# Performance work log

Measured on AMD Instinct MI355X. Metric: run time of the kernel, lower is better.

## Reference

```python
import jax, jax.numpy as jnp
import numpy as np

EPS = 1e-12
BETA = 3.0
N_TH = 21


def setup_inputs() -> dict:
    key = jax.random.key(0)
    k1, k2 = jax.random.split(key)
    N, C = 65536, 1000
    logits = jax.random.normal(k1, (N, C), dtype=jnp.float32)
    labels = jax.random.randint(k2, (N,), 0, C, dtype=jnp.int64)
    idx = jnp.arange(N, dtype=jnp.int64)
    return {"logits": logits, "labels": labels, "idx": idx, "type": 0}


def _forward(logits, labels):
    # probs / confidences / predictions
    probs = jax.nn.softmax(logits, axis=1)                      # [N, C]
    conf = jnp.max(probs, axis=1)                               # [N]
    preds = jnp.argmax(probs, axis=1)                           # [N]
    # predictive uncertainty (type == 0): entropy of softmax
    unc = -jnp.sum(probs * jnp.log(probs + EPS), axis=-1)       # [N]
    umin, umax = jnp.min(unc), jnp.max(unc)
    th = jnp.linspace(0.0, 1.0, N_TH, dtype=logits.dtype)       # [21]
    unc_th = umin + th * (umax - umin)                          # [21]

    acc = (labels == preds)                                     # [N] bool
    t_unc = jnp.tanh(unc)                                       # [N]
    certain = unc[None, :] <= unc_th[:, None]                   # [21, N]
    a = acc[None, :]

    zero = jnp.zeros((), logits.dtype)
    n_ac = jnp.sum(jnp.where(a & certain, conf * (1.0 - t_unc), zero), axis=1)
    n_au = jnp.sum(jnp.where(a & ~certain, conf * t_unc, zero), axis=1)
    n_ic = jnp.sum(jnp.where(~a & certain, (1.0 - conf) * (1.0 - t_unc), zero), axis=1)
    n_iu = jnp.sum(jnp.where(~a & ~certain, (1.0 - conf) * t_unc, zero), axis=1)

    avu = (n_ac + n_iu) / (n_ac + n_au + n_ic + n_iu + EPS)     # [21]
    # sklearn.metrics.auc == trapezoidal rule over (th, avu)
    auc_avu = 0.5 * jnp.sum((avu[1:] + avu[:-1]) * (th[1:] - th[:-1]))
    # original wraps auc in a fresh tensor -> no grad through the AvU branch
    avu_loss = -BETA * jnp.log(jax.lax.stop_gradient(auc_avu) + EPS)

    logp = jax.nn.log_softmax(logits, axis=1)                   # [N, C]
    ce = -jnp.mean(jnp.take_along_axis(logp, labels[:, None], axis=1))
    return (avu_loss + ce)[None]                                # [1], matches torch


def reference(logits, labels, idx, type) -> jnp.ndarray:
    del idx, type  # idx unused; type=0 path (predictive uncertainty)
    return _forward(logits, labels)
```

## Files before the change

### kernel.cpp

```cpp
#include <hip/hip_runtime.h>
#include <math.h>

#define NROWS 65536
#define NC    1000
#define NTH   21

__device__ __forceinline__ void upd_max(float v, int i, float& m, int& mi) {
    if (v > m) { m = v; mi = i; }
}

__global__ void k0_init(float* bins, float* ce_sum, unsigned* umin_b, unsigned* umax_b) {
    int i = threadIdx.x;
    if (i < 88) bins[i] = 0.f;
    if (i == 88) *ce_sum = 0.f;
    if (i == 89) *umin_b = 0x7f800000u;
    if (i == 90) *umax_b = 0u;
}

__global__ __launch_bounds__(256) void k1_rowstats(
        const float* __restrict__ logits, const int* __restrict__ labels,
        float* __restrict__ unc_o, float* __restrict__ confs_o, float* __restrict__ logp_o)
{
    const int wave = threadIdx.x >> 6;
    const int lane = threadIdx.x & 63;
    const int row  = (blockIdx.x << 2) + wave;
    const float4* rp = (const float4*)(logits + (size_t)row * NC);

    float4 r0 = rp[lane];
    float4 r1 = rp[lane + 64];
    float4 r2 = rp[lane + 128];
    float4 r3 = make_float4(-1e30f, -1e30f, -1e30f, -1e30f);
    if (lane < 250 - 192) r3 = rp[lane + 192];

    float m = -1e30f; int mi = 0;
    int b0 = lane << 2;
    upd_max(r0.x, b0 + 0, m, mi); upd_max(r0.y, b0 + 1, m, mi);
    upd_max(r0.z, b0 + 2, m, mi); upd_max(r0.w, b0 + 3, m, mi);
    int b1 = (lane + 64) << 2;
    upd_max(r1.x, b1 + 0, m, mi); upd_max(r1.y, b1 + 1, m, mi);
    upd_max(r1.z, b1 + 2, m, mi); upd_max(r1.w, b1 + 3, m, mi);
    int b2 = (lane + 128) << 2;
    upd_max(r2.x, b2 + 0, m, mi); upd_max(r2.y, b2 + 1, m, mi);
    upd_max(r2.z, b2 + 2, m, mi); upd_max(r2.w, b2 + 3, m, mi);
    int b3 = (lane + 192) << 2;
    upd_max(r3.x, b3 + 0, m, mi); upd_max(r3.y, b3 + 1, m, mi);
    upd_max(r3.z, b3 + 2, m, mi); upd_max(r3.w, b3 + 3, m, mi);

    #pragma unroll
    for (int off = 1; off < 64; off <<= 1) {
        float om = __shfl_xor(m, off, 64);
        int   oi = __shfl_xor(mi, off, 64);
        if (om > m || (om == m && oi < mi)) { m = om; mi = oi; }
    }

    float se = 0.f, sx = 0.f;
#define ACCUM(v) { float t_ = (v) - m; float e_ = __expf(t_); se += e_; sx = fmaf(e_, t_, sx); }
    ACCUM(r0.x) ACCUM(r0.y) ACCUM(r0.z) ACCUM(r0.w)
    ACCUM(r1.x) ACCUM(r1.y) ACCUM(r1.z) ACCUM(r1.w)
    ACCUM(r2.x) ACCUM(r2.y) ACCUM(r2.z) ACCUM(r2.w)
    ACCUM(r3.x) ACCUM(r3.y) ACCUM(r3.z) ACCUM(r3.w)
#undef ACCUM
    #pragma unroll
    for (int off = 1; off < 64; off <<= 1) {
        se += __shfl_xor(se, off, 64);
        sx += __shfl_xor(sx, off, 64);
    }

    float Z    = se;
    float logZ = logf(Z);
    float conf = 1.0f / Z;
    float uncv = logZ - sx / Z;

    int label = labels[row];
    int f4 = label >> 2, slot = label & 3, it = f4 >> 6;
    float4 q = (it == 0) ? r0 : (it == 1) ? r1 : (it == 2) ? r2 : r3;
    float cand = (slot == 0) ? q.x : (slot == 1) ? q.y : (slot == 2) ? q.z : q.w;
    float xl = __shfl(cand, f4 & 63, 64);

    if (lane == 0) {
        unc_o[row]   = uncv;
        confs_o[row] = (mi == label) ? conf : -conf;
        logp_o[row]  = (xl - m) - logZ;
    }
}

__global__ __launch_bounds__(256) void k2_reduce(
        const float* __restrict__ unc, const float* __restrict__ logp,
        float* ce_sum, unsigned* umin_b, unsigned* umax_b)
{
    float mn = 1e30f, mx = -1e30f, s = 0.f;
    for (int i = blockIdx.x * 256 + threadIdx.x; i < NROWS; i += 256 * gridDim.x) {
        float u = unc[i];
        mn = fminf(mn, u); mx = fmaxf(mx, u); s += logp[i];
    }
    #pragma unroll
    for (int off = 1; off < 64; off <<= 1) {
        mn = fminf(mn, __shfl_xor(mn, off, 64));
        mx = fmaxf(mx, __shfl_xor(mx, off, 64));
        s += __shfl_xor(s, off, 64);
    }
    __shared__ float smn[4], smx[4], ss[4];
    int wave = threadIdx.x >> 6;
    if ((threadIdx.x & 63) == 0) { smn[wave] = mn; smx[wave] = mx; ss[wave] = s; }
    __syncthreads();
    if (threadIdx.x == 0) {
        mn = fminf(fminf(smn[0], smn[1]), fminf(smn[2], smn[3]));
        mx = fmaxf(fmaxf(smx[0], smx[1]), fmaxf(smx[2], smx[3]));
        s  = ss[0] + ss[1] + ss[2] + ss[3];
        atomicAdd(ce_sum, s);
        atomicMin(umin_b, __float_as_uint(mn));
        atomicMax(umax_b, __float_as_uint(mx));
    }
}

__global__ __launch_bounds__(256) void k3_hist(
        const float* __restrict__ unc, const float* __restrict__ confs,
        const unsigned* __restrict__ umin_b, const unsigned* __restrict__ umax_b,
        float* __restrict__ bins)
{
    __shared__ float h[88];
    for (int i = threadIdx.x; i < 88; i += 256) h[i] = 0.f;
    __syncthreads();
    float umin = __uint_as_float(*umin_b);
    float umax = __uint_as_float(*umax_b);
    float du = umax - umin;

    int i = blockIdx.x * 256 + threadIdx.x;
    float u  = unc[i];
    float cs = confs[i];
    float conf = fabsf(cs);
    bool  acc  = cs > 0.f;
    float tu = tanhf(u);

    int b = NTH;
    #pragma unroll
    for (int t = NTH - 1; t >= 0; --t) {
        float th = umin + ((float)t * 0.05f) * du;
        if (u <= th) b = t;
    }
    float w = acc ? conf : (1.f - conf);
    int base = acc ? 0 : 44;
    atomicAdd(&h[base + b],       w * (1.f - tu));
    atomicAdd(&h[base + 22 + b],  w * tu);
    __syncthreads();
    for (int i2 = threadIdx.x; i2 < 88; i2 += 256) {
        float v = h[i2];
        if (v != 0.f) atomicAdd(&bins[i2], v);
    }
}

__global__ void k4_final(const float* __restrict__ bins, const float* __restrict__ ce_sum,
                         float* __restrict__ out)
{
    if (threadIdx.x != 0 || blockIdx.x != 0) return;
    float tot_au = 0.f, tot_iu = 0.f;
    for (int b = 0; b < 22; ++b) { tot_au += bins[22 + b]; tot_iu += bins[66 + b]; }
    float cac = 0.f, cau = 0.f, cic = 0.f, ciu = 0.f;
    float avu[NTH];
    for (int t = 0; t < NTH; ++t) {
        cac += bins[t]; cau += bins[22 + t]; cic += bins[44 + t]; ciu += bins[66 + t];
        float nac = cac, nau = tot_au - cau, nic = cic, niu = tot_iu - ciu;
        avu[t] = (nac + niu) / (nac + nau + nic + niu + 1e-12f);
    }
    float auc = 0.f;
    for (int t = 0; t + 1 < NTH; ++t) auc += 0.5f * (avu[t + 1] + avu[t]) * 0.05f;
    float avu_loss = -3.0f * logf(auc + 1e-12f);
    float ce = -(*ce_sum) / (float)NROWS;
    out[0] = avu_loss + ce;
}

extern "C" void kernel_launch(void* const* d_in, const int* in_sizes, int n_in,
                              void* d_out, int out_size, void* d_ws, size_t ws_size,
                              hipStream_t stream)
{
    const float* logits = (const float*)d_in[0];
    const int*   labels = (const int*)d_in[1];
    float* ws    = (float*)d_ws;
    float* unc   = ws;
    float* confs = ws + NROWS;
    float* logp  = ws + 2 * NROWS;
    float* bins  = ws + 3 * NROWS;
    float* ce_sum = bins + 88;
    unsigned* umin_b = (unsigned*)(ce_sum + 1);
    unsigned* umax_b = umin_b + 1;

    hipLaunchKernelGGL(k0_init, dim3(1), dim3(128), 0, stream, bins, ce_sum, umin_b, umax_b);
    hipLaunchKernelGGL(k1_rowstats, dim3(NROWS / 4), dim3(256), 0, stream,
                       logits, labels, unc, confs, logp);
    hipLaunchKernelGGL(k2_reduce, dim3(256), dim3(256), 0, stream,
                       unc, logp, ce_sum, umin_b, umax_b);
    hipLaunchKernelGGL(k3_hist, dim3(NROWS / 256), dim3(256), 0, stream,
                       unc, confs, umin_b, umax_b, bins);
    hipLaunchKernelGGL(k4_final, dim3(1), dim3(64), 0, stream,
                       bins, ce_sum, (float*)d_out);
}
```

Baseline: 370.2 us.

## Fold min/max/CE reduction into rowstats and drop global atomics and init kernel

Each rowstats block now writes its own min, max and CE partial, which removes the separate reduction kernel and the init kernel. The histogram kernel re-reduces the 16K block partials in every one of its 64 blocks and writes per-block histograms instead of using global atomics. The final kernel sums the CE partials and the histograms. This cuts the launch count from five to three and avoids atomic contention, at the cost of redundant partial reads in each histogram block.

```diff
diff --git a/kernel.cpp b/kernel.cpp
--- a/kernel.cpp
+++ b/kernel.cpp
@@ -1,25 +1,21 @@
 #include <hip/hip_runtime.h>
 #include <math.h>
 
-#define NROWS 65536
-#define NC    1000
-#define NTH   21
+#define NROWS   65536
+#define NC      1000
+#define NTH     21
+#define K1_BLKS (NROWS / 4)
+#define H_BLKS  64
+#define NBINS   22
 
 __device__ __forceinline__ void upd_max(float v, int i, float& m, int& mi) {
     if (v > m) { m = v; mi = i; }
 }
 
-__global__ void k0_init(float* bins, float* ce_sum, unsigned* umin_b, unsigned* umax_b) {
-    int i = threadIdx.x;
-    if (i < 88) bins[i] = 0.f;
-    if (i == 88) *ce_sum = 0.f;
-    if (i == 89) *umin_b = 0x7f800000u;
-    if (i == 90) *umax_b = 0u;
-}
-
 __global__ __launch_bounds__(256) void k1_rowstats(
         const float* __restrict__ logits, const int* __restrict__ labels,
-        float* __restrict__ unc_o, float* __restrict__ confs_o, float* __restrict__ logp_o)
+        float* __restrict__ unc_o, float* __restrict__ confs_o,
+        float* __restrict__ pmin, float* __restrict__ pmax, float* __restrict__ pce)
 {
     const int wave = threadIdx.x >> 6;
     const int lane = threadIdx.x & 63;
@@ -76,56 +72,61 @@
     float4 q = (it == 0) ? r0 : (it == 1) ? r1 : (it == 2) ? r2 : r3;
     float cand = (slot == 0) ? q.x : (slot == 1) ? q.y : (slot == 2) ? q.z : q.w;
     float xl = __shfl(cand, f4 & 63, 64);
-
+    float logp = (xl - m) - logZ;
+
+    __shared__ float s_u[4], s_lp[4];
     if (lane == 0) {
         unc_o[row]   = uncv;
         confs_o[row] = (mi == label) ? conf : -conf;
-        logp_o[row]  = (xl - m) - logZ;
-    }
-}
-
-__global__ __launch_bounds__(256) void k2_reduce(
-        const float* __restrict__ unc, const float* __restrict__ logp,
-        float* ce_sum, unsigned* umin_b, unsigned* umax_b)
-{
-    float mn = 1e30f, mx = -1e30f, s = 0.f;
-    for (int i = blockIdx.x * 256 + threadIdx.x; i < NROWS; i += 256 * gridDim.x) {
-        float u = unc[i];
-        mn = fminf(mn, u); mx = fmaxf(mx, u); s += logp[i];
+        s_u[wave] = uncv; s_lp[wave] = logp;
+    }
+    __syncthreads();
+    if (threadIdx.x == 0) {
+        float mn = fminf(fminf(s_u[0], s_u[1]), fminf(s_u[2], s_u[3]));
+        float mx = fmaxf(fmaxf(s_u[0], s_u[1]), fmaxf(s_u[2], s_u[3]));
+        pmin[blockIdx.x] = mn;
+        pmax[blockIdx.x] = mx;
+        pce[blockIdx.x]  = s_lp[0] + s_lp[1] + s_lp[2] + s_lp[3];
+    }
+}
+
+__global__ __launch_bounds__(1024) void k3_hist(
+        const float* __restrict__ unc, const float* __restrict__ confs,
+        const float* __restrict__ pmin, const float* __restrict__ pmax,
+        float* __restrict__ hist)
+{
+    __shared__ float h[4 * NBINS];
+    __shared__ float smn[16], smx[16];
+    __shared__ float s_umin, s_umax;
+    const int tid  = threadIdx.x;
+    const int wave = tid >> 6;
+    const int lane = tid & 63;
+
+    float mn = 1e30f, mx = -1e30f;
+    #pragma unroll
+    for (int t = 0; t < K1_BLKS / 1024; ++t) {
+        int i = tid + t * 1024;
+        mn = fminf(mn, pmin[i]);
+        mx = fmaxf(mx, pmax[i]);
     }
     #pragma unroll
     for (int off = 1; off < 64; off <<= 1) {
         mn = fminf(mn, __shfl_xor(mn, off, 64));
         mx = fmaxf(mx, __shfl_xor(mx, off, 64));
-        s += __shfl_xor(s, off, 64);
-    }
-    __shared__ float smn[4], smx[4], ss[4];
-    int wave = threadIdx.x >> 6;
-    if ((threadIdx.x & 63) == 0) { smn[wave] = mn; smx[wave] = mx; ss[wave] = s; }
-    __syncthreads();
-    if (threadIdx.x == 0) {
-        mn = fminf(fminf(smn[0], smn[1]), fminf(smn[2], smn[3]));
-        mx = fmaxf(fmaxf(smx[0], smx[1]), fmaxf(smx[2], smx[3]));
-        s  = ss[0] + ss[1] + ss[2] + ss[3];
-        atomicAdd(ce_sum, s);
-        atomicMin(umin_b, __float_as_uint(mn));
-        atomicMax(umax_b, __float_as_uint(mx));
-    }
-}
-
-__global__ __launch_bounds__(256) void k3_hist(
-        const float* __restrict__ unc, const float* __restrict__ confs,
-        const unsigned* __restrict__ umin_b, const unsigned* __restrict__ umax_b,
-        float* __restrict__ bins)
-{
-    __shared__ float h[88];
-    for (int i = threadIdx.x; i < 88; i += 256) h[i] = 0.f;
-    __syncthreads();
-    float umin = __uint_as_float(*umin_b);
-    float umax = __uint_as_float(*umax_b);
-    float du = umax - umin;
-
-    int i = blockIdx.x * 256 + threadIdx.x;
+    }
+    if (lane == 0) { smn[wave] = mn; smx[wave] = mx; }
+    if (tid < 4 * NBINS) h[tid] = 0.f;
+    __syncthreads();
+    if (tid == 0) {
+        float a = 1e30f, b = -1e30f;
+        #pragma unroll
+        for (int w = 0; w < 16; ++w) { a = fminf(a, smn[w]); b = fmaxf(b, smx[w]); }
+        s_umin = a; s_umax = b;
+    }
+    __syncthreads();
+    float umin = s_umin, du = s_umax - s_umin;
+
+    int i = blockIdx.x * 1024 + tid;
     float u  = unc[i];
     float cs = confs[i];
     float conf = fabsf(cs);
@@ -139,34 +140,54 @@
         if (u <= th) b = t;
     }
     float w = acc ? conf : (1.f - conf);
-    int base = acc ? 0 : 44;
-    atomicAdd(&h[base + b],       w * (1.f - tu));
-    atomicAdd(&h[base + 22 + b],  w * tu);
-    __syncthreads();
-    for (int i2 = threadIdx.x; i2 < 88; i2 += 256) {
-        float v = h[i2];
-        if (v != 0.f) atomicAdd(&bins[i2], v);
-    }
-}
-
-__global__ void k4_final(const float* __restrict__ bins, const float* __restrict__ ce_sum,
-                         float* __restrict__ out)
-{
-    if (threadIdx.x != 0 || blockIdx.x != 0) return;
-    float tot_au = 0.f, tot_iu = 0.f;
-    for (int b = 0; b < 22; ++b) { tot_au += bins[22 + b]; tot_iu += bins[66 + b]; }
-    float cac = 0.f, cau = 0.f, cic = 0.f, ciu = 0.f;
-    float avu[NTH];
-    for (int t = 0; t < NTH; ++t) {
-        cac += bins[t]; cau += bins[22 + t]; cic += bins[44 + t]; ciu += bins[66 + t];
-        float nac = cac, nau = tot_au - cau, nic = cic, niu = tot_iu - ciu;
-        avu[t] = (nac + niu) / (nac + nau + nic + niu + 1e-12f);
-    }
-    float auc = 0.f;
-    for (int t = 0; t + 1 < NTH; ++t) auc += 0.5f * (avu[t + 1] + avu[t]) * 0.05f;
-    float avu_loss = -3.0f * logf(auc + 1e-12f);
-    float ce = -(*ce_sum) / (float)NROWS;
-    out[0] = avu_loss + ce;
+    int base = acc ? 0 : 2 * NBINS;
+    atomicAdd(&h[base + b],         w * (1.f - tu));
+    atomicAdd(&h[base + NBINS + b], w * tu);
+    __syncthreads();
+    if (tid < 4 * NBINS) hist[blockIdx.x * 4 * NBINS + tid] = h[tid];
+}
+
+__global__ __launch_bounds__(256) void k4_final(
+        const float* __restrict__ pce, const float* __restrict__ hist,
+        float* __restrict__ out)
+{
+    const int tid = threadIdx.x;
+    float s = 0.f;
+    for (int i = tid; i < K1_BLKS; i += 256) s += pce[i];
+    #pragma unroll
+    for (int off = 1; off < 64; off <<= 1) s += __shfl_xor(s, off, 64);
+    __shared__ float ss[4];
+    if ((tid & 63) == 0) ss[tid >> 6] = s;
+    __shared__ float bins[4 * NBINS];
+    if (tid < 4 * NBINS) {
+        float v = 0.f;
+        for (int blk = 0; blk < H_BLKS; ++blk) v += hist[blk * 4 * NBINS + tid];
+        bins[tid] = v;
+    }
+    __syncthreads();
+    if (tid == 0) {
+        float ce_sum = ss[0] + ss[1] + ss[2] + ss[3];
+        float tot_au = 0.f, tot_iu = 0.f;
+        for (int b = 0; b < NBINS; ++b) {
+            tot_au += bins[NBINS + b];
+            tot_iu += bins[3 * NBINS + b];
+        }
+        float cac = 0.f, cau = 0.f, cic = 0.f, ciu = 0.f;
+        float avu[NTH];
+        for (int t = 0; t < NTH; ++t) {
+            cac += bins[t];
+            cau += bins[NBINS + t];
+            cic += bins[2 * NBINS + t];
+            ciu += bins[3 * NBINS + t];
+            float nac = cac, nau = tot_au - cau, nic = cic, niu = tot_iu - ciu;
+            avu[t] = (nac + niu) / (nac + nau + nic + niu + 1e-12f);
+        }
+        float auc = 0.f;
+        for (int t = 0; t + 1 < NTH; ++t) auc += 0.5f * (avu[t + 1] + avu[t]) * 0.05f;
+        float avu_loss = -3.0f * logf(auc + 1e-12f);
+        float ce = -ce_sum / (float)NROWS;
+        out[0] = avu_loss + ce;
+    }
 }
 
 extern "C" void kernel_launch(void* const* d_in, const int* in_sizes, int n_in,
@@ -177,20 +198,16 @@
     const int*   labels = (const int*)d_in[1];
     float* ws    = (float*)d_ws;
     float* unc   = ws;
-    float* confs = ws + NROWS;
-    float* logp  = ws + 2 * NROWS;
-    float* bins  = ws + 3 * NROWS;
-    float* ce_sum = bins + 88;
-    unsigned* umin_b = (unsigned*)(ce_sum + 1);
-    unsigned* umax_b = umin_b + 1;
-
-    hipLaunchKernelGGL(k0_init, dim3(1), dim3(128), 0, stream, bins, ce_sum, umin_b, umax_b);
-    hipLaunchKernelGGL(k1_rowstats, dim3(NROWS / 4), dim3(256), 0, stream,
-                       logits, labels, unc, confs, logp);
-    hipLaunchKernelGGL(k2_reduce, dim3(256), dim3(256), 0, stream,
-                       unc, logp, ce_sum, umin_b, umax_b);
-    hipLaunchKernelGGL(k3_hist, dim3(NROWS / 256), dim3(256), 0, stream,
-                       unc, confs, umin_b, umax_b, bins);
-    hipLaunchKernelGGL(k4_final, dim3(1), dim3(64), 0, stream,
-                       bins, ce_sum, (float*)d_out);
-}
+    float* confs = unc + NROWS;
+    float* pmin  = confs + NROWS;
+    float* pmax  = pmin + K1_BLKS;
+    float* pce   = pmax + K1_BLKS;
+    float* hist  = pce + K1_BLKS;
+
+    hipLaunchKernelGGL(k1_rowstats, dim3(K1_BLKS), dim3(256), 0, stream,
+                       logits, labels, unc, confs, pmin, pmax, pce);
+    hipLaunchKernelGGL(k3_hist, dim3(H_BLKS), dim3(1024), 0, stream,
+                       unc, confs, pmin, pmax, hist);
+    hipLaunchKernelGGL(k4_final, dim3(1), dim3(256), 0, stream,
+                       pce, hist, (float*)d_out);
+}
```

Measured after the change: 374.5 us. No clear change (+1.1%).
